# Optimization experiments

Hardware: AMD Instinct MI355X
Metric: run time of the kernel (lower is better)

Reference implementation:

```python
import jax, jax.numpy as jnp
import numpy as np

HEADS = 16

def setup_inputs() -> dict:
    key = jax.random.key(0)
    k1, k2, k3 = jax.random.split(key, 3)
    B, S, D = 4, 2048, 1024
    x = jax.random.normal(k1, (B, S, D), dtype=jnp.float32)
    w_qkv = jax.random.normal(k2, (D, 3 * D), dtype=jnp.float32) * (D ** -0.5)
    w_out = jax.random.normal(k3, (D, D), dtype=jnp.float32) * (D ** -0.5)
    return {"x": x, "w_qkv": w_qkv, "w_out": w_out}

def reference(x, w_qkv, w_out):
    B, S, D = x.shape
    H = HEADS
    hd = D // H
    qkv = jnp.einsum("bsd,de->bse", x, w_qkv)  # [B,S,3D]
    q, k, v = jnp.split(qkv, 3, axis=-1)
    # [B,S,D] -> [B,H,S,hd]
    q = q.reshape(B, S, H, hd).transpose(0, 2, 1, 3)
    k = k.reshape(B, S, H, hd).transpose(0, 2, 1, 3)
    v = v.reshape(B, S, H, hd).transpose(0, 2, 1, 3)
    scores = jnp.einsum("bhqd,bhkd->bhqk", q, k) / jnp.sqrt(jnp.float32(hd))
    attn = jax.nn.softmax(scores, axis=-1)
    out = jnp.einsum("bhqk,bhkd->bhqd", attn, v)  # [B,H,S,hd]
    out = out.transpose(0, 2, 1, 3).reshape(B, S, D)
    return jnp.einsum("bsd,de->bse", out, w_out)
```

## Files before the change

kernel.cpp:

```cpp
#include <hip/hip_runtime.h>

typedef __bf16 bf16;
typedef __bf16 bfx8 __attribute__((ext_vector_type(8)));
typedef __bf16 bfx4 __attribute__((ext_vector_type(4)));
typedef float f32x4 __attribute__((ext_vector_type(4)));

#define MFMA_BF16 __builtin_amdgcn_mfma_f32_16x16x32_bf16

static constexpr int Bq = 4, Sq = 2048, Dq = 1024, Hq = 16, HDq = 64;
static constexpr int Mq = Bq * Sq;
static constexpr int D3 = 3 * Dq;
static constexpr int NQK = 2 * Dq;
static constexpr float L2E = 1.4426950408889634f;
static constexpr float QSC = 0.125f * L2E;

typedef const __attribute__((address_space(1))) void* gas1;
typedef __attribute__((address_space(3))) void* las3;

__device__ __forceinline__ void gload_lds16(const bf16* g, bf16* l) {
    __builtin_amdgcn_global_load_lds((gas1)g, (las3)l, 16, 0, 0);
}

__device__ __forceinline__ float fast_exp2(float x) {
    return __builtin_amdgcn_exp2f(x);
}

__global__ __launch_bounds__(256) void prep(const float* __restrict__ x,
                                            const float* __restrict__ w_qkv,
                                            const float* __restrict__ w_out,
                                            bf16* __restrict__ x_bf,
                                            bf16* __restrict__ wqkvT,
                                            bf16* __restrict__ woutT) {
    __shared__ float tile[32][33];
    int bid = blockIdx.x, tid = threadIdx.x;
    if (bid < 8192) {
        int i = (bid * 256 + tid) * 4;
        float4 v = *(const float4*)(x + i);
        bfx4 r;
        r[0] = (bf16)v.x; r[1] = (bf16)v.y; r[2] = (bf16)v.z; r[3] = (bf16)v.w;
        *(bfx4*)(x_bf + i) = r;
        return;
    }
    const float* in; bf16* out; int R, C, blk;
    if (bid < 8192 + 3072) { blk = bid - 8192;  in = w_qkv; out = wqkvT; R = Dq; C = D3; }
    else                   { blk = bid - 11264; in = w_out; out = woutT; R = Dq; C = Dq; }
    int tx = tid & 31, ty = tid >> 5;
    int nbx = C / 32;
    int c0 = (blk % nbx) * 32, r0 = (blk / nbx) * 32;
    for (int j = 0; j < 32; j += 8)
        tile[ty + j][tx] = in[(size_t)(r0 + ty + j) * C + c0 + tx];
    __syncthreads();
    for (int j = 0; j < 32; j += 8)
        out[(size_t)(c0 + ty + j) * R + r0 + tx] = (bf16)tile[tx][ty + j];
}

__device__ __forceinline__ int ldsb(int d, int s) {
    return d * 256 + ((((s >> 3) ^ (d & 15)) << 4) | ((s & 7) * 2));
}

template <bool OUT_F32, bool QSCALE, bool VSPLIT>
__global__ __launch_bounds__(256) void gemm_bt(const bf16* __restrict__ A,
                                               const bf16* __restrict__ Bt,
                                               void* __restrict__ Cout,
                                               bf16* __restrict__ Vout,
                                               int M, int N, int K) {
    __shared__ bf16 smem[2 * 8192];
    bf16* As = smem;
    bf16* Bs = smem + 8192;
    int m0 = blockIdx.y * 128;
    int n0 = blockIdx.x * 128;
    int tid = threadIdx.x;
    int lane = tid & 63, wave = tid >> 6;
    int quad = lane >> 4, l16 = lane & 15;
    int wr = wave >> 1, wc = wave & 1;
    int sw = l16 & 7;

    f32x4 acc[4][4] = {};

    for (int k0 = 0; k0 < K; k0 += 64) {
        __syncthreads();
        #pragma unroll
        for (int i = 0; i < 4; i++) {
            int c = i * 256 + tid;
            int row = c >> 3;
            int ch = (c & 7) ^ (row & 7);
            gload_lds16(A + (size_t)(m0 + row) * K + k0 + ch * 8, As + c * 8);
            gload_lds16(Bt + (size_t)(n0 + row) * K + k0 + ch * 8, Bs + c * 8);
        }
        __syncthreads();
        #pragma unroll
        for (int s = 0; s < 2; s++) {
            bfx8 af[4], bfr[4];
            #pragma unroll
            for (int i = 0; i < 4; i++)
                af[i] = *(const bfx8*)(As + (wr * 64 + i * 16 + l16) * 64 +
                                       ((s * 4 + quad) ^ sw) * 8);
            #pragma unroll
            for (int j = 0; j < 4; j++)
                bfr[j] = *(const bfx8*)(Bs + (wc * 64 + j * 16 + l16) * 64 +
                                        ((s * 4 + quad) ^ sw) * 8);
            #pragma unroll
            for (int i = 0; i < 4; i++)
                #pragma unroll
                for (int j = 0; j < 4; j++)
                    acc[i][j] = MFMA_BF16(af[i], bfr[j], acc[i][j], 0, 0, 0);
        }
    }

    if (VSPLIT && n0 >= NQK) {
        __syncthreads();
        #pragma unroll
        for (int i = 0; i < 4; i++)
            #pragma unroll
            for (int j = 0; j < 4; j++) {
                int d = wc * 64 + j * 16 + l16;
                int s0 = wr * 64 + i * 16 + quad * 4;
                bfx4 pv;
                #pragma unroll
                for (int r = 0; r < 4; r++) pv[r] = (bf16)acc[i][j][r];
                *(bfx4*)((char*)smem + ldsb(d, s0)) = pv;
            }
        __syncthreads();
        int b = m0 >> 11, st = m0 & (Sq - 1), d0 = n0 - NQK;
        int g = (lane >> 3) & 1, t8 = lane & 7;
        int ss = g * 64 + (t8 >> 2) * 32 + (t8 & 3) * 4;
        #pragma unroll
        for (int rep = 0; rep < 8; rep++) {
            int d = wave * 4 + (lane >> 4) + rep * 16;
            bfx4 lo = *(const bfx4*)((char*)smem + ldsb(d, ss));
            bfx4 hi = *(const bfx4*)((char*)smem + ldsb(d, ss + 16));
            bfx8 o8;
            #pragma unroll
            for (int r = 0; r < 4; r++) { o8[r] = lo[r]; o8[4 + r] = hi[r]; }
            *(bfx8*)(Vout + ((size_t)b * Dq + d0 + d) * Sq + st + g * 64 + t8 * 8) = o8;
        }
        return;
    }

    #pragma unroll
    for (int i = 0; i < 4; i++)
        #pragma unroll
        for (int j = 0; j < 4; j++) {
            int col = n0 + wc * 64 + j * 16 + l16;
            int cstride = VSPLIT ? NQK : N;
            float scale = (QSCALE && col < Dq) ? QSC : 1.0f;
            #pragma unroll
            for (int r = 0; r < 4; r++) {
                int row = m0 + wr * 64 + i * 16 + quad * 4 + r;
                if (OUT_F32)
                    ((float*)Cout)[(size_t)row * cstride + col] = acc[i][j][r];
                else
                    ((bf16*)Cout)[(size_t)row * cstride + col] = (bf16)(acc[i][j][r] * scale);
            }
        }
}

__global__ __launch_bounds__(256, 4) void attn_kernel(const bf16* __restrict__ qkv,
                                                      const bf16* __restrict__ Vt,
                                                      bf16* __restrict__ out) {
    __shared__ bf16 Ks[2][64 * 64];
    __shared__ bf16 Vs[2][64 * 64];

    int bid = blockIdx.x;
    int qc = (bid >> 3) & 15;
    int head = ((bid >> 7) << 3) | (bid & 7);
    int h = head & 15, b = head >> 4;
    int tid = threadIdx.x;
    int lane = tid & 63, wave = tid >> 6;
    int quad = lane >> 4, l16 = lane & 15;
    int sw = l16 & 7;

    size_t base = (size_t)b * Sq * NQK;
    const bf16* Kbase = qkv + base + Dq + h * HDq;
    const bf16* Vbase = Vt + ((size_t)b * Dq + h * HDq) * Sq;
    int q0 = qc * 128 + wave * 32;

    bfx8 qf[2][2];
    #pragma unroll
    for (int qt = 0; qt < 2; qt++)
        #pragma unroll
        for (int s = 0; s < 2; s++)
            qf[qt][s] = *(const bfx8*)(qkv + base + (size_t)(q0 + qt * 16 + l16) * NQK +
                                       h * HDq + s * 32 + quad * 8);

    bfx8 ones;
    #pragma unroll
    for (int j = 0; j < 8; j++) ones[j] = (bf16)1.0f;

    f32x4 oacc[2][4] = {};
    f32x4 lacc[2] = {};

    int c0 = tid, c1 = tid + 256;
    int r0 = c0 >> 3, ch0 = (c0 & 7) ^ (r0 & 7);
    int r1 = c1 >> 3, ch1 = (c1 & 7) ^ (r1 & 7);

    gload_lds16(Kbase + (size_t)r0 * NQK + ch0 * 8, Ks[0] + c0 * 8);
    gload_lds16(Vbase + (size_t)r0 * Sq + ch0 * 8, Vs[0] + c0 * 8);
    gload_lds16(Kbase + (size_t)r1 * NQK + ch1 * 8, Ks[0] + c1 * 8);
    gload_lds16(Vbase + (size_t)r1 * Sq + ch1 * 8, Vs[0] + c1 * 8);

    for (int i = 0; i < 32; i++) {
        int cur = i & 1;
        __syncthreads();
        if (i + 1 < 32) {
            int k0 = (i + 1) * 64;
            bf16* kd = Ks[cur ^ 1];
            bf16* vd = Vs[cur ^ 1];
            gload_lds16(Kbase + (size_t)(k0 + r0) * NQK + ch0 * 8, kd + c0 * 8);
            gload_lds16(Vbase + (size_t)r0 * Sq + k0 + ch0 * 8, vd + c0 * 8);
            gload_lds16(Kbase + (size_t)(k0 + r1) * NQK + ch1 * 8, kd + c1 * 8);
            gload_lds16(Vbase + (size_t)r1 * Sq + k0 + ch1 * 8, vd + c1 * 8);
        }
        const bf16* K_ = Ks[cur];
        const bf16* V_ = Vs[cur];

        #pragma unroll
        for (int hf = 0; hf < 2; hf++) {
            bfx8 kf[2][2];
            #pragma unroll
            for (int tp = 0; tp < 2; tp++) {
                int krow = ((2 * hf + tp) * 16 + l16) * 64;
                kf[tp][0] = *(const bfx8*)(K_ + krow + (quad ^ sw) * 8);
                kf[tp][1] = *(const bfx8*)(K_ + krow + ((4 + quad) ^ sw) * 8);
            }

            bfx8 pf[2];
            #pragma unroll
            for (int qt = 0; qt < 2; qt++) {
                f32x4 s0 = {}, s1 = {};
                s0 = MFMA_BF16(kf[0][0], qf[qt][0], s0, 0, 0, 0);
                s0 = MFMA_BF16(kf[0][1], qf[qt][1], s0, 0, 0, 0);
                s1 = MFMA_BF16(kf[1][0], qf[qt][0], s1, 0, 0, 0);
                s1 = MFMA_BF16(kf[1][1], qf[qt][1], s1, 0, 0, 0);
                bfx8 p;
                #pragma unroll
                for (int r = 0; r < 4; r++) {
                    p[r]     = (bf16)fast_exp2(s0[r]);
                    p[4 + r] = (bf16)fast_exp2(s1[r]);
                }
                pf[qt] = p;
                lacc[qt] = MFMA_BF16(pf[qt], ones, lacc[qt], 0, 0, 0);
            }

            #pragma unroll
            for (int nt = 0; nt < 4; nt++) {
                bfx8 vf = *(const bfx8*)(V_ + (nt * 16 + l16) * 64 +
                                         ((hf * 4 + quad) ^ sw) * 8);
                oacc[0][nt] = MFMA_BF16(pf[0], vf, oacc[0][nt], 0, 0, 0);
                oacc[1][nt] = MFMA_BF16(pf[1], vf, oacc[1][nt], 0, 0, 0);
            }
        }
    }

    #pragma unroll
    for (int qt = 0; qt < 2; qt++)
        #pragma unroll
        for (int r = 0; r < 4; r++) {
            int row = q0 + qt * 16 + quad * 4 + r;
            float inv = 1.0f / lacc[qt][r];
            #pragma unroll
            for (int nt = 0; nt < 4; nt++)
                out[((size_t)b * Sq + row) * Dq + h * HDq + nt * 16 + l16] =
                    (bf16)(oacc[qt][nt][r] * inv);
        }
}

extern "C" void kernel_launch(void* const* d_in, const int* in_sizes, int n_in,
                              void* d_out, int out_size, void* d_ws, size_t ws_size,
                              hipStream_t stream) {
    const float* x     = (const float*)d_in[0];
    const float* w_qkv = (const float*)d_in[1];
    const float* w_out = (const float*)d_in[2];
    float* out = (float*)d_out;

    char* ws = (char*)d_ws;
    bf16* x_bf   = (bf16*)ws;
    bf16* wqkvT  = (bf16*)(ws + 16777216);
    bf16* woutT  = (bf16*)(ws + 16777216 + 6291456);
    bf16* qkv2   = (bf16*)(ws + 25165824);
    bf16* Vt     = (bf16*)(ws + 25165824 + 33554432);
    bf16* attn   = x_bf;

    prep<<<8192 + 3072 + 1024, 256, 0, stream>>>(x, w_qkv, w_out, x_bf, wqkvT, woutT);

    gemm_bt<false, true, true><<<dim3(D3 / 128, Mq / 128), 256, 0, stream>>>(
        x_bf, wqkvT, qkv2, Vt, Mq, D3, Dq);

    attn_kernel<<<1024, 256, 0, stream>>>(qkv2, Vt, attn);

    gemm_bt<true, false, false><<<dim3(Dq / 128, Mq / 128), 256, 0, stream>>>(
        attn, woutT, out, nullptr, Mq, Dq, Dq);
}
```

Measured before the change: 252.0 us.

## Software-pipeline attention: overlap PV MFMAs of previous tile with QK and exp

New measurement: 257.3 us. 2.1% more time.

```diff
diff --git a/kernel.cpp b/kernel.cpp
--- a/kernel.cpp
+++ b/kernel.cpp
@@ -159,7 +159,7 @@
                                                       const bf16* __restrict__ Vt,
                                                       bf16* __restrict__ out) {
     __shared__ bf16 Ks[2][64 * 64];
-    __shared__ bf16 Vs[2][64 * 64];
+    __shared__ bf16 Vs[3][64 * 64];
 
     int bid = blockIdx.x;
     int qc = (bid >> 3) & 15;
@@ -189,33 +189,34 @@
 
     f32x4 oacc[2][4] = {};
     f32x4 lacc[2] = {};
+    bfx8 pfp[2][2];
 
     int c0 = tid, c1 = tid + 256;
     int r0 = c0 >> 3, ch0 = (c0 & 7) ^ (r0 & 7);
     int r1 = c1 >> 3, ch1 = (c1 & 7) ^ (r1 & 7);
 
+    bf16 *vP = Vs[2], *vC = Vs[0], *vN = Vs[1];
+
     gload_lds16(Kbase + (size_t)r0 * NQK + ch0 * 8, Ks[0] + c0 * 8);
-    gload_lds16(Vbase + (size_t)r0 * Sq + ch0 * 8, Vs[0] + c0 * 8);
+    gload_lds16(Vbase + (size_t)r0 * Sq + ch0 * 8, vC + c0 * 8);
     gload_lds16(Kbase + (size_t)r1 * NQK + ch1 * 8, Ks[0] + c1 * 8);
-    gload_lds16(Vbase + (size_t)r1 * Sq + ch1 * 8, Vs[0] + c1 * 8);
+    gload_lds16(Vbase + (size_t)r1 * Sq + ch1 * 8, vC + c1 * 8);
 
     for (int i = 0; i < 32; i++) {
-        int cur = i & 1;
         __syncthreads();
         if (i + 1 < 32) {
             int k0 = (i + 1) * 64;
-            bf16* kd = Ks[cur ^ 1];
-            bf16* vd = Vs[cur ^ 1];
+            bf16* kd = Ks[(i + 1) & 1];
             gload_lds16(Kbase + (size_t)(k0 + r0) * NQK + ch0 * 8, kd + c0 * 8);
-            gload_lds16(Vbase + (size_t)r0 * Sq + k0 + ch0 * 8, vd + c0 * 8);
+            gload_lds16(Vbase + (size_t)r0 * Sq + k0 + ch0 * 8, vN + c0 * 8);
             gload_lds16(Kbase + (size_t)(k0 + r1) * NQK + ch1 * 8, kd + c1 * 8);
-            gload_lds16(Vbase + (size_t)r1 * Sq + k0 + ch1 * 8, vd + c1 * 8);
-        }
-        const bf16* K_ = Ks[cur];
-        const bf16* V_ = Vs[cur];
-
-        #pragma unroll
-        for (int hf = 0; hf < 2; hf++) {
+            gload_lds16(Vbase + (size_t)r1 * Sq + k0 + ch1 * 8, vN + c1 * 8);
+        }
+        const bf16* K_ = Ks[i & 1];
+
+        f32x4 sc[2][2][2];
+        #pragma unroll
+        for (int hf = 0; hf < 1; hf++) {
             bfx8 kf[2][2];
             #pragma unroll
             for (int tp = 0; tp < 2; tp++) {
@@ -223,8 +224,6 @@
                 kf[tp][0] = *(const bfx8*)(K_ + krow + (quad ^ sw) * 8);
                 kf[tp][1] = *(const bfx8*)(K_ + krow + ((4 + quad) ^ sw) * 8);
             }
-
-            bfx8 pf[2];
             #pragma unroll
             for (int qt = 0; qt < 2; qt++) {
                 f32x4 s0 = {}, s1 = {};
@@ -232,23 +231,71 @@
                 s0 = MFMA_BF16(kf[0][1], qf[qt][1], s0, 0, 0, 0);
                 s1 = MFMA_BF16(kf[1][0], qf[qt][0], s1, 0, 0, 0);
                 s1 = MFMA_BF16(kf[1][1], qf[qt][1], s1, 0, 0, 0);
+                sc[hf][qt][0] = s0; sc[hf][qt][1] = s1;
+            }
+        }
+
+        if (i > 0) {
+            #pragma unroll
+            for (int hf = 0; hf < 2; hf++) {
+                lacc[0] = MFMA_BF16(pfp[hf][0], ones, lacc[0], 0, 0, 0);
+                lacc[1] = MFMA_BF16(pfp[hf][1], ones, lacc[1], 0, 0, 0);
+                #pragma unroll
+                for (int nt = 0; nt < 4; nt++) {
+                    bfx8 vf = *(const bfx8*)(vP + (nt * 16 + l16) * 64 +
+                                             ((hf * 4 + quad) ^ sw) * 8);
+                    oacc[0][nt] = MFMA_BF16(pfp[hf][0], vf, oacc[0][nt], 0, 0, 0);
+                    oacc[1][nt] = MFMA_BF16(pfp[hf][1], vf, oacc[1][nt], 0, 0, 0);
+                }
+            }
+        }
+
+        #pragma unroll
+        for (int hf = 1; hf < 2; hf++) {
+            bfx8 kf[2][2];
+            #pragma unroll
+            for (int tp = 0; tp < 2; tp++) {
+                int krow = ((2 * hf + tp) * 16 + l16) * 64;
+                kf[tp][0] = *(const bfx8*)(K_ + krow + (quad ^ sw) * 8);
+                kf[tp][1] = *(const bfx8*)(K_ + krow + ((4 + quad) ^ sw) * 8);
+            }
+            #pragma unroll
+            for (int qt = 0; qt < 2; qt++) {
+                f32x4 s0 = {}, s1 = {};
+                s0 = MFMA_BF16(kf[0][0], qf[qt][0], s0, 0, 0, 0);
+                s0 = MFMA_BF16(kf[0][1], qf[qt][1], s0, 0, 0, 0);
+                s1 = MFMA_BF16(kf[1][0], qf[qt][0], s1, 0, 0, 0);
+                s1 = MFMA_BF16(kf[1][1], qf[qt][1], s1, 0, 0, 0);
+                sc[hf][qt][0] = s0; sc[hf][qt][1] = s1;
+            }
+        }
+
+        #pragma unroll
+        for (int hf = 0; hf < 2; hf++)
+            #pragma unroll
+            for (int qt = 0; qt < 2; qt++) {
                 bfx8 p;
                 #pragma unroll
                 for (int r = 0; r < 4; r++) {
-                    p[r]     = (bf16)fast_exp2(s0[r]);
-                    p[4 + r] = (bf16)fast_exp2(s1[r]);
+                    p[r]     = (bf16)fast_exp2(sc[hf][qt][0][r]);
+                    p[4 + r] = (bf16)fast_exp2(sc[hf][qt][1][r]);
                 }
-                pf[qt] = p;
-                lacc[qt] = MFMA_BF16(pf[qt], ones, lacc[qt], 0, 0, 0);
-            }
-
-            #pragma unroll
-            for (int nt = 0; nt < 4; nt++) {
-                bfx8 vf = *(const bfx8*)(V_ + (nt * 16 + l16) * 64 +
-                                         ((hf * 4 + quad) ^ sw) * 8);
-                oacc[0][nt] = MFMA_BF16(pf[0], vf, oacc[0][nt], 0, 0, 0);
-                oacc[1][nt] = MFMA_BF16(pf[1], vf, oacc[1][nt], 0, 0, 0);
-            }
+                pfp[hf][qt] = p;
+            }
+
+        bf16* t = vP; vP = vC; vC = vN; vN = t;
+    }
+
+    #pragma unroll
+    for (int hf = 0; hf < 2; hf++) {
+        lacc[0] = MFMA_BF16(pfp[hf][0], ones, lacc[0], 0, 0, 0);
+        lacc[1] = MFMA_BF16(pfp[hf][1], ones, lacc[1], 0, 0, 0);
+        #pragma unroll
+        for (int nt = 0; nt < 4; nt++) {
+            bfx8 vf = *(const bfx8*)(vP + (nt * 16 + l16) * 64 +
+                                     ((hf * 4 + quad) ^ sw) * 8);
+            oacc[0][nt] = MFMA_BF16(pfp[hf][0], vf, oacc[0][nt], 0, 0, 0);
+            oacc[1][nt] = MFMA_BF16(pfp[hf][1], vf, oacc[1][nt], 0, 0, 0);
         }
     }
 
```

## Triple-buffer K tiles with explicit vmcnt waits in attention loop

Applied to the files above, without the earlier changes.

Result: faster. 244.3 us (-3.1%).

```diff
diff --git a/kernel.cpp b/kernel.cpp
--- a/kernel.cpp
+++ b/kernel.cpp
@@ -158,7 +158,7 @@
 __global__ __launch_bounds__(256, 4) void attn_kernel(const bf16* __restrict__ qkv,
                                                       const bf16* __restrict__ Vt,
                                                       bf16* __restrict__ out) {
-    __shared__ bf16 Ks[2][64 * 64];
+    __shared__ bf16 Ks[3][64 * 64];
     __shared__ bf16 Vs[2][64 * 64];
 
     int bid = blockIdx.x;
@@ -194,25 +194,33 @@
     int r0 = c0 >> 3, ch0 = (c0 & 7) ^ (r0 & 7);
     int r1 = c1 >> 3, ch1 = (c1 & 7) ^ (r1 & 7);
 
-    gload_lds16(Kbase + (size_t)r0 * NQK + ch0 * 8, Ks[0] + c0 * 8);
-    gload_lds16(Vbase + (size_t)r0 * Sq + ch0 * 8, Vs[0] + c0 * 8);
-    gload_lds16(Kbase + (size_t)r1 * NQK + ch1 * 8, Ks[0] + c1 * 8);
-    gload_lds16(Vbase + (size_t)r1 * Sq + ch1 * 8, Vs[0] + c1 * 8);
-
+    bf16 *kC = Ks[0], *kN = Ks[1], *kF = Ks[2];
+    bf16 *vC = Vs[0], *vN = Vs[1];
+
+    gload_lds16(Kbase + (size_t)r0 * NQK + ch0 * 8, kC + c0 * 8);
+    gload_lds16(Kbase + (size_t)r1 * NQK + ch1 * 8, kC + c1 * 8);
+    gload_lds16(Vbase + (size_t)r0 * Sq + ch0 * 8, vC + c0 * 8);
+    gload_lds16(Vbase + (size_t)r1 * Sq + ch1 * 8, vC + c1 * 8);
+    gload_lds16(Kbase + (size_t)(64 + r0) * NQK + ch0 * 8, kN + c0 * 8);
+    gload_lds16(Kbase + (size_t)(64 + r1) * NQK + ch1 * 8, kN + c1 * 8);
+
+    #pragma unroll 1
     for (int i = 0; i < 32; i++) {
-        int cur = i & 1;
-        __syncthreads();
+        if (i < 31) asm volatile("s_waitcnt vmcnt(2)" ::: "memory");
+        else        asm volatile("s_waitcnt vmcnt(0)" ::: "memory");
+        __builtin_amdgcn_s_barrier();
         if (i + 1 < 32) {
             int k0 = (i + 1) * 64;
-            bf16* kd = Ks[cur ^ 1];
-            bf16* vd = Vs[cur ^ 1];
-            gload_lds16(Kbase + (size_t)(k0 + r0) * NQK + ch0 * 8, kd + c0 * 8);
-            gload_lds16(Vbase + (size_t)r0 * Sq + k0 + ch0 * 8, vd + c0 * 8);
-            gload_lds16(Kbase + (size_t)(k0 + r1) * NQK + ch1 * 8, kd + c1 * 8);
-            gload_lds16(Vbase + (size_t)r1 * Sq + k0 + ch1 * 8, vd + c1 * 8);
-        }
-        const bf16* K_ = Ks[cur];
-        const bf16* V_ = Vs[cur];
+            gload_lds16(Vbase + (size_t)r0 * Sq + k0 + ch0 * 8, vN + c0 * 8);
+            gload_lds16(Vbase + (size_t)r1 * Sq + k0 + ch1 * 8, vN + c1 * 8);
+        }
+        if (i + 2 < 32) {
+            int k0 = (i + 2) * 64;
+            gload_lds16(Kbase + (size_t)(k0 + r0) * NQK + ch0 * 8, kF + c0 * 8);
+            gload_lds16(Kbase + (size_t)(k0 + r1) * NQK + ch1 * 8, kF + c1 * 8);
+        }
+        const bf16* K_ = kC;
+        const bf16* V_ = vC;
 
         #pragma unroll
         for (int hf = 0; hf < 2; hf++) {
@@ -250,6 +258,9 @@
                 oacc[1][nt] = MFMA_BF16(pf[1], vf, oacc[1][nt], 0, 0, 0);
             }
         }
+
+        bf16* kt = kC; kC = kN; kN = kF; kF = kt;
+        bf16* vt = vC; vC = vN; vN = vt;
     }
 
     #pragma unroll
```
